# Kernel tuning notes

Measured on AMD Instinct MI355X. Metric: run time of the kernel, lower is better.

## Reference

```python
import jax, jax.numpy as jnp
import numpy as np
import math


def _instance_norm(x, eps=1e-5):
    # x: [B,C,H,W], normalize over spatial dims per (b,c)
    mu = jnp.mean(x, axis=(2, 3), keepdims=True)
    var = jnp.var(x, axis=(2, 3), keepdims=True)
    return (x - mu) * jax.lax.rsqrt(var + eps)


def _conv1x1(x, W, b):
    # x: [B,C,H,W], W: [O,C], b: [O]
    return jnp.einsum('oc,bchw->bohw', W, x) + b[None, :, None, None]


def setup_inputs() -> dict:
    key = jax.random.key(0)
    ks = jax.random.split(key, 17)
    B, C, H, W = 4, 256, 128, 128
    x = jax.random.normal(ks[0], (B, C, H, W), jnp.float32)
    def w(k):
        return jax.random.normal(k, (C, C), jnp.float32) * 0.02
    def bias(k):
        return jax.random.normal(k, (C,), jnp.float32) * 0.02
    return {
        'x': x,
        'Wq1': w(ks[1]), 'bq1': bias(ks[2]),
        'Wq2': w(ks[3]), 'bq2': bias(ks[4]),
        'Wk1': w(ks[5]), 'bk1': bias(ks[6]),
        'Wk2': w(ks[7]), 'bk2': bias(ks[8]),
        'Wv': w(ks[9]), 'bv': bias(ks[10]),
        'Wg': w(ks[11]), 'bg': bias(ks[12]),
        'Wo': w(ks[13]), 'bo': bias(ks[14]),
    }


def reference(x, Wq1, bq1, Wq2, bq2, Wk1, bk1, Wk2, bk2, Wv, bv, Wg, bg, Wo, bo):
    B, C, H, W = x.shape
    N = H * W
    sqrtC = math.sqrt(C)

    xn = _instance_norm(x)
    gelu = lambda t: jax.nn.gelu(t, approximate=False)

    q = jax.nn.softplus(_conv1x1(gelu(_conv1x1(xn, Wq1, bq1)), Wq2, bq2))
    k = jax.nn.softplus(_conv1x1(gelu(_conv1x1(xn, Wk1, bk1)), Wk2, bk2))
    v = gelu(_conv1x1(xn, Wv, bv))
    g = gelu(_conv1x1(xn, Wg, bg))

    q = q.reshape(B, C, N).transpose(0, 2, 1)  # [B,N,C]
    k = k.reshape(B, C, N)                     # [B,C,N]
    v = v.reshape(B, C, N).transpose(0, 2, 1)  # [B,N,C]

    kv = jnp.einsum('bcn,bnd->bcd', k, v)               # [B,C,C]
    z = jnp.einsum('bnc,bc->bn', q, k.sum(axis=-1)) / sqrtC
    z = 1.0 / (z + N)                                   # [B,N]

    out = jnp.einsum('bnc,bcd->bnd', q, kv) / sqrtC + v  # [B,N,C]
    out = out * z[:, :, None]
    out = out.transpose(0, 2, 1).reshape(B, C, H, W)
    out = out * g
    out = _conv1x1(out, Wo, bo)
    return out
```

## Files before the change

### kernel.cpp

```cpp
#include <hip/hip_runtime.h>
#include <cstdint>
#include <cstddef>


#define DI __device__ __forceinline__

typedef __attribute__((ext_vector_type(8))) short bf16x8;
typedef __attribute__((ext_vector_type(4))) short bf16x4;
typedef __attribute__((ext_vector_type(4))) float f32x4;

static constexpr int Cc = 256;
static constexpr int NN = 16384;

DI float bf2f(short s){ unsigned int u = ((unsigned int)(unsigned short)s) << 16; float f; __builtin_memcpy(&f, &u, 4); return f; }
DI short f2bf(float f){ unsigned int u; __builtin_memcpy(&u, &f, 4); u += 0x7fffu + ((u >> 16) & 1u); return (short)(u >> 16); }

typedef __attribute__((address_space(1))) const unsigned int gu32;
typedef __attribute__((address_space(3))) unsigned int lu32;
DI void gload16(const short* g, short* l){
    __builtin_amdgcn_global_load_lds((gu32*)g, (lu32*)l, 16, 0, 0);
}

DI float geluf(float x){
    float zz = x * 0.70710678118654752f;
    float az = fabsf(zz);
    float t  = __builtin_amdgcn_rcpf(fmaf(0.3275911f, az, 1.0f));
    float p  = fmaf(fmaf(fmaf(fmaf(1.061405429f, t, -1.453152027f), t,
                   1.421413741f), t, -0.284496736f), t, 0.254829592f) * t;
    float e  = __expf(-az * az);
    float er = copysignf(1.0f - p * e, zz);
    return 0.5f * x * (1.0f + er);
}
DI float softplusf(float x){
    float e = __expf(-fabsf(x));
    return fmaxf(x, 0.0f) + __logf(1.0f + e);
}

__global__ __launch_bounds__(256) void tw_conv(
    const float* __restrict__ W0, const float* __restrict__ W1,
    const float* __restrict__ W2, const float* __restrict__ W3,
    const float* __restrict__ W4, const float* __restrict__ W5,
    const float* __restrict__ W6, short* __restrict__ dst)
{
    const float* srcs[7] = {W0, W1, W2, W3, W4, W5, W6};
    const float* W = srcs[blockIdx.y];
    short* d = dst + (size_t)blockIdx.y * 65536;
    int i = blockIdx.x * 256 + threadIdx.x;
    float4 v = *(const float4*)(W + (size_t)i * 4);
    bf16x4 pk = { f2bf(v.x), f2bf(v.y), f2bf(v.z), f2bf(v.w) };
    *(bf16x4*)(d + (size_t)i * 4) = pk;
}

__global__ __launch_bounds__(256) void t0_stats(const float* __restrict__ x,
                                                float* __restrict__ mu, float* __restrict__ rstd)
{
    int row = blockIdx.x;
    const float4* p = (const float4*)(x + (size_t)row * NN);
    float s = 0.f, ss = 0.f;
    for (int i = threadIdx.x; i < NN/4; i += 256){
        float4 v = p[i];
        s  += v.x + v.y + v.z + v.w;
        ss += v.x*v.x + v.y*v.y + v.z*v.z + v.w*v.w;
    }
    #pragma unroll
    for (int o = 32; o; o >>= 1){ s += __shfl_down(s, o); ss += __shfl_down(ss, o); }
    __shared__ float a0[4], a1[4];
    int w = threadIdx.x >> 6;
    if ((threadIdx.x & 63) == 0){ a0[w] = s; a1[w] = ss; }
    __syncthreads();
    if (threadIdx.x == 0){
        float S = a0[0]+a0[1]+a0[2]+a0[3], SS = a1[0]+a1[1]+a1[2]+a1[3];
        float m = S * (1.f/NN);
        float var = SS * (1.f/NN) - m*m;
        mu[row] = m;
        rstd[row] = rsqrtf(var + 1e-5f);
    }
}

__global__ __launch_bounds__(256) void t1_xnT(const float* __restrict__ x,
                                              const float* __restrict__ mu, const float* __restrict__ rstd,
                                              short* __restrict__ xnT)
{
    int n0 = blockIdx.x * 64, c0 = blockIdx.y * 64, b = blockIdx.z;
    __shared__ __align__(16) short lds[64*72];
    int t = threadIdx.x;
    #pragma unroll
    for (int i = 0; i < 4; i++){
        int idx = i*256 + t;
        int c  = idx >> 4;
        int n4 = idx & 15;
        int cg = b*Cc + c0 + c;
        float4 v = *(const float4*)(x + (size_t)cg*NN + n0 + n4*4);
        float m = mu[cg], rs = rstd[cg];
        int key = (c ^ (c >> 3)) & 7;
        int blk = (n4 >> 1) ^ key;
        bf16x4 pk = { f2bf((v.x-m)*rs), f2bf((v.y-m)*rs), f2bf((v.z-m)*rs), f2bf((v.w-m)*rs) };
        *(bf16x4*)(&lds[c*72 + blk*8 + (n4&1)*4]) = pk;
    }
    __syncthreads();
    #pragma unroll
    for (int i = 0; i < 2; i++){
        int idx = i*256 + t;
        int n  = idx >> 3;
        int c8 = idx & 7;
        bf16x8 pk;
        #pragma unroll
        for (int j = 0; j < 8; j++){
            int c = c8*8 + j;
            int key = (c ^ (c >> 3)) & 7;
            pk[j] = lds[c*72 + (((n >> 3) ^ key))*8 + (n & 7)];
        }
        *(bf16x8*)(xnT + ((size_t)(b*NN + n0 + n))*Cc + c0 + c8*8) = pk;
    }
}

__global__ __launch_bounds__(256) void t2_conv1(const short* __restrict__ xnT,
    const short* __restrict__ wbf,
    const float* __restrict__ bv, const float* __restrict__ bg,
    short* __restrict__ yvg)
{
    int n0 = blockIdx.x * 128;
    int stile = blockIdx.y;
    int b = blockIdx.z;
    int branch = 2 + (stile >> 1);
    const short* wb = wbf + (size_t)branch * 65536;
    const float* bs = (stile >> 1) ? bg : bv;
    int s0b = (stile & 1) * 128;
    int dcol = stile * 128;

    __shared__ __align__(16) short Al[128*32];
    __shared__ __align__(16) short Bl[128*32];
    int t = threadIdx.x, lane = t & 63, wid = t >> 6;
    int wm = (wid & 1) * 64, wn = (wid >> 1) * 64;
    int l15 = lane & 15, g = lane >> 4;
    int srow = wid*16 + (lane >> 2);
    int scol = (lane & 3) * 8;
    int sdst = wid*512 + lane*8;

    f32x4 acc[4][4];
    #pragma unroll
    for (int i=0;i<4;i++)
        #pragma unroll
        for (int j=0;j<4;j++){ acc[i][j][0]=0.f; acc[i][j][1]=0.f; acc[i][j][2]=0.f; acc[i][j][3]=0.f; }

    const short* xb = xnT + (size_t)(b*NN + n0) * Cc;

    for (int k0 = 0; k0 < 256; k0 += 32){
        __syncthreads();
        #pragma unroll
        for (int i = 0; i < 2; i++){
            gload16(xb + (size_t)(i*64 + srow)*Cc + k0 + scol, &Al[i*2048 + sdst]);
            gload16(wb + (size_t)(s0b + i*64 + srow)*Cc + k0 + scol, &Bl[i*2048 + sdst]);
        }
        __syncthreads();
        bf16x8 bfr[4];
        #pragma unroll
        for (int ni = 0; ni < 4; ni++) bfr[ni] = *(const bf16x8*)(&Bl[(wn + ni*16 + l15)*32 + g*8]);
        #pragma unroll
        for (int mi = 0; mi < 4; mi++){
            bf16x8 a = *(const bf16x8*)(&Al[(wm + mi*16 + l15)*32 + g*8]);
            #pragma unroll
            for (int ni = 0; ni < 4; ni++)
                acc[mi][ni] = __builtin_amdgcn_mfma_f32_16x16x32_bf16(a, bfr[ni], acc[mi][ni], 0, 0, 0);
        }
    }
    short* outb = yvg + (size_t)(b*NN + n0) * 512 + dcol;
    #pragma unroll
    for (int mi = 0; mi < 4; mi++)
        #pragma unroll
        for (int ni = 0; ni < 4; ni++){
            int coll = wn + ni*16 + l15;
            float bias = bs[s0b + coll];
            #pragma unroll
            for (int r = 0; r < 4; r++){
                int row = wm + mi*16 + g*4 + r;
                outb[(size_t)row*512 + coll] = f2bf(geluf(acc[mi][ni][r] + bias));
            }
        }
}

__global__ __launch_bounds__(256) void t23_fused(const short* __restrict__ xnT,
    const short* __restrict__ wbf,
    const float* __restrict__ bq1, const float* __restrict__ bk1,
    const float* __restrict__ bq2, const float* __restrict__ bk2,
    short* __restrict__ qkT, float* __restrict__ ksum)
{
    int n0 = blockIdx.x * 64;
    int branch = blockIdx.y;
    int b = blockIdx.z;
    const short* w1 = wbf + (size_t)branch * 65536;
    const short* w2 = wbf + (size_t)(4 + branch) * 65536;
    const float* bs1 = branch ? bk1 : bq1;
    const float* bs2 = branch ? bk2 : bq2;

    __shared__ __align__(16) short Al[64*32];
    __shared__ __align__(16) short Bl[256*32];
    __shared__ __align__(16) short Y1[64*264];
    int t = threadIdx.x, lane = t & 63, wid = t >> 6;
    int wn = wid * 64;
    int l15 = lane & 15, g = lane >> 4;
    int srowA = t >> 2, scolA = (t & 3) * 8, sdstA = t * 8;
    int srowB = wid*16 + (lane >> 2);
    int scolB = (lane & 3) * 8;
    int sdstB = wid*512 + lane*8;

    const short* xb = xnT + (size_t)(b*NN + n0) * Cc;

    f32x4 acc[4][4];
    #pragma unroll
    for (int i=0;i<4;i++)
        #pragma unroll
        for (int j=0;j<4;j++){ acc[i][j][0]=0.f; acc[i][j][1]=0.f; acc[i][j][2]=0.f; acc[i][j][3]=0.f; }

    for (int k0 = 0; k0 < 256; k0 += 32){
        __syncthreads();
        gload16(xb + (size_t)srowA*Cc + k0 + scolA, &Al[sdstA]);
        #pragma unroll
        for (int i = 0; i < 4; i++)
            gload16(w1 + (size_t)(i*64 + srowB)*Cc + k0 + scolB, &Bl[i*2048 + sdstB]);
        __syncthreads();
        bf16x8 bfr[4];
        #pragma unroll
        for (int ni = 0; ni < 4; ni++) bfr[ni] = *(const bf16x8*)(&Bl[(wn + ni*16 + l15)*32 + g*8]);
        #pragma unroll
        for (int mi = 0; mi < 4; mi++){
            bf16x8 a = *(const bf16x8*)(&Al[(mi*16 + l15)*32 + g*8]);
            #pragma unroll
            for (int ni = 0; ni < 4; ni++)
                acc[mi][ni] = __builtin_amdgcn_mfma_f32_16x16x32_bf16(a, bfr[ni], acc[mi][ni], 0, 0, 0);
        }
    }
    #pragma unroll
    for (int mi = 0; mi < 4; mi++)
        #pragma unroll
        for (int ni = 0; ni < 4; ni++){
            int coll = wn + ni*16 + l15;
            float bias = bs1[coll];
            #pragma unroll
            for (int r = 0; r < 4; r++){
                int row = mi*16 + g*4 + r;
                Y1[row*264 + coll] = f2bf(geluf(acc[mi][ni][r] + bias));
            }
        }

    f32x4 acc2[4][4];
    #pragma unroll
    for (int i=0;i<4;i++)
        #pragma unroll
        for (int j=0;j<4;j++){ acc2[i][j][0]=0.f; acc2[i][j][1]=0.f; acc2[i][j][2]=0.f; acc2[i][j][3]=0.f; }

    for (int k0 = 0; k0 < 256; k0 += 32){
        __syncthreads();
        #pragma unroll
        for (int i = 0; i < 4; i++)
            gload16(w2 + (size_t)(i*64 + srowB)*Cc + k0 + scolB, &Bl[i*2048 + sdstB]);
        __syncthreads();
        bf16x8 bfr[4];
        #pragma unroll
        for (int ni = 0; ni < 4; ni++) bfr[ni] = *(const bf16x8*)(&Bl[(wn + ni*16 + l15)*32 + g*8]);
        #pragma unroll
        for (int mi = 0; mi < 4; mi++){
            bf16x8 a = *(const bf16x8*)(&Y1[(mi*16 + l15)*264 + k0 + g*8]);
            #pragma unroll
            for (int ni = 0; ni < 4; ni++)
                acc2[mi][ni] = __builtin_amdgcn_mfma_f32_16x16x32_bf16(a, bfr[ni], acc2[mi][ni], 0, 0, 0);
        }
    }
    short* outb = qkT + (size_t)(b*NN + n0) * 512 + branch*256;
    float csum[4] = {0.f, 0.f, 0.f, 0.f};
    #pragma unroll
    for (int mi = 0; mi < 4; mi++)
        #pragma unroll
        for (int ni = 0; ni < 4; ni++){
            int coll = wn + ni*16 + l15;
            float bias = bs2[coll];
            #pragma unroll
            for (int r = 0; r < 4; r++){
                int row = mi*16 + g*4 + r;
                float val = softplusf(acc2[mi][ni][r] + bias);
                outb[(size_t)row*512 + coll] = f2bf(val);
                csum[ni] += val;
            }
        }
    if (branch == 1){
        #pragma unroll
        for (int ni = 0; ni < 4; ni++){
            float v = csum[ni];
            v += __shfl_xor(v, 16);
            v += __shfl_xor(v, 32);
            if (g == 0) atomicAdd(&ksum[b*Cc + wn + ni*16 + l15], v);
        }
    }
}

__global__ __launch_bounds__(256) void t3t_transpose(const short* __restrict__ qkT, const short* __restrict__ yvg,
                                                     short* __restrict__ kC, short* __restrict__ vC)
{
    int n0 = blockIdx.x * 64;
    int c0 = blockIdx.y * 64;
    int b  = blockIdx.z >> 1;
    int which = blockIdx.z & 1;
    const short* src; short* dst;
    if (which == 0){ src = qkT + (size_t)(b*NN + n0)*512 + 256 + c0; dst = kC + (size_t)(b*Cc + c0)*NN + n0; }
    else           { src = yvg + (size_t)(b*NN + n0)*512 +   0 + c0; dst = vC + (size_t)(b*Cc + c0)*NN + n0; }
    __shared__ __align__(16) short lds[64*72];
    int t = threadIdx.x;
    #pragma unroll
    for (int i = 0; i < 2; i++){
        int idx = i*256 + t;
        int n = idx >> 3, c8 = idx & 7;
        bf16x8 v = *(const bf16x8*)(src + (size_t)n*512 + c8*8);
        int key = (n ^ (n >> 3)) & 7;
        *(bf16x8*)(&lds[n*72 + (c8 ^ key)*8]) = v;
    }
    __syncthreads();
    #pragma unroll
    for (int i = 0; i < 2; i++){
        int idx = i*256 + t;
        int c = idx >> 3, n8 = idx & 7;
        bf16x8 pk;
        #pragma unroll
        for (int j = 0; j < 8; j++){
            int n = n8*8 + j;
            int key = (n ^ (n >> 3)) & 7;
            pk[j] = lds[n*72 + (((c >> 3) ^ key))*8 + (c & 7)];
        }
        *(bf16x8*)(dst + (size_t)c*NN + n8*8) = pk;
    }
}

__global__ __launch_bounds__(256) void t4_kv(const short* __restrict__ kC, const short* __restrict__ vC,
                                             float* __restrict__ kv)
{
    int m0 = blockIdx.x * 128;
    int d0 = blockIdx.y * 128;
    int b  = blockIdx.z >> 5;
    int nb = (blockIdx.z & 31) * 512;

    __shared__ __align__(16) short Al[128*32];
    __shared__ __align__(16) short Bl[128*32];
    int t = threadIdx.x, lane = t & 63, wid = t >> 6;
    int wm = (wid & 1) * 64, wn = (wid >> 1) * 64;
    int l15 = lane & 15, g = lane >> 4;
    int srow = wid*16 + (lane >> 2);
    int scol = (lane & 3) * 8;
    int sdst = wid*512 + lane*8;

    f32x4 acc[4][4];
    #pragma unroll
    for (int i=0;i<4;i++)
        #pragma unroll
        for (int j=0;j<4;j++){ acc[i][j][0]=0.f; acc[i][j][1]=0.f; acc[i][j][2]=0.f; acc[i][j][3]=0.f; }

    const short* ka = kC + (size_t)(b*Cc + m0)*NN + nb;
    const short* vb = vC + (size_t)(b*Cc + d0)*NN + nb;

    for (int k0 = 0; k0 < 512; k0 += 32){
        __syncthreads();
        #pragma unroll
        for (int i = 0; i < 2; i++){
            gload16(ka + (size_t)(i*64 + srow)*NN + k0 + scol, &Al[i*2048 + sdst]);
            gload16(vb + (size_t)(i*64 + srow)*NN + k0 + scol, &Bl[i*2048 + sdst]);
        }
        __syncthreads();
        bf16x8 bfr[4];
        #pragma unroll
        for (int ni = 0; ni < 4; ni++) bfr[ni] = *(const bf16x8*)(&Bl[(wn + ni*16 + l15)*32 + g*8]);
        #pragma unroll
        for (int mi = 0; mi < 4; mi++){
            bf16x8 a = *(const bf16x8*)(&Al[(wm + mi*16 + l15)*32 + g*8]);
            #pragma unroll
            for (int ni = 0; ni < 4; ni++)
                acc[mi][ni] = __builtin_amdgcn_mfma_f32_16x16x32_bf16(a, bfr[ni], acc[mi][ni], 0, 0, 0);
        }
    }
    #pragma unroll
    for (int mi = 0; mi < 4; mi++)
        #pragma unroll
        for (int ni = 0; ni < 4; ni++){
            int coll = wn + ni*16 + l15;
            #pragma unroll
            for (int r = 0; r < 4; r++){
                int row = wm + mi*16 + g*4 + r;
                atomicAdd(&kv[((size_t)b*Cc + m0 + row)*Cc + d0 + coll], acc[mi][ni][r]);
            }
        }
}

__global__ __launch_bounds__(256) void t4c_kvT(const float* __restrict__ kv, short* __restrict__ kvT16)
{
    int d = blockIdx.x, b = blockIdx.y, c = threadIdx.x;
    float v = kv[((size_t)b*Cc + c)*Cc + d] * 0.0625f;
    kvT16[((size_t)b*Cc + d)*Cc + c] = f2bf(v);
}

__global__ __launch_bounds__(256) void t5_z(const short* __restrict__ qkT, const float* __restrict__ ksum,
                                            float* __restrict__ z)
{
    int b = blockIdx.y;
    int n0 = blockIdx.x * 32;
    __shared__ float ks[256];
    int t = threadIdx.x;
    ks[t] = ksum[b*Cc + t];
    __syncthreads();
    int row = n0 + (t >> 3), l8 = t & 7;
    const short* q = qkT + (size_t)(b*NN + row)*512;
    float acc = 0.f;
    #pragma unroll
    for (int i = 0; i < 4; i++){
        int c8 = i*8 + l8;
        bf16x8 v = *(const bf16x8*)(q + c8*8);
        #pragma unroll
        for (int j = 0; j < 8; j++) acc += bf2f(v[j]) * ks[c8*8 + j];
    }
    acc += __shfl_down(acc, 4, 8);
    acc += __shfl_down(acc, 2, 8);
    acc += __shfl_down(acc, 1, 8);
    if (l8 == 0) z[b*NN + row] = 1.0f / (acc * 0.0625f + 16384.0f);
}

__global__ __launch_bounds__(256) void t6_final(const short* __restrict__ qkT, const short* __restrict__ kvT16,
    const short* __restrict__ yvg, const float* __restrict__ z,
    const short* __restrict__ wbf, const float* __restrict__ bo, float* __restrict__ out)
{
    int n0 = blockIdx.x * 64, b = blockIdx.y;
    __shared__ __align__(16) short Aq[64*32];
    __shared__ __align__(16) short Bw[256*32];
    __shared__ __align__(16) short S[64*264];
    int t = threadIdx.x, lane = t & 63, wid = t >> 6;
    int l15 = lane & 15, g = lane >> 4;
    const short* wo_bf = wbf + (size_t)6 * 65536;
    int srow = wid*16 + (lane >> 2);
    int scol = (lane & 3) * 8;
    int sdst = wid*512 + lane*8;

    f32x4 acc[4][4];
    #pragma unroll
    for (int i=0;i<4;i++)
        #pragma unroll
        for (int j=0;j<4;j++){ acc[i][j][0]=0.f; acc[i][j][1]=0.f; acc[i][j][2]=0.f; acc[i][j][3]=0.f; }

    const short* qb = qkT + (size_t)(b*NN + n0)*512;
    const short* kvb = kvT16 + (size_t)b*Cc*Cc;

    for (int k0 = 0; k0 < 256; k0 += 32){
        __syncthreads();
        gload16(qb + (size_t)srow*512 + k0 + scol, &Aq[sdst]);
        #pragma unroll
        for (int i = 0; i < 4; i++)
            gload16(kvb + (size_t)(i*64 + srow)*Cc + k0 + scol, &Bw[i*2048 + sdst]);
        __syncthreads();
        bf16x8 bfr[4];
        #pragma unroll
        for (int ni = 0; ni < 4; ni++) bfr[ni] = *(const bf16x8*)(&Bw[(wid*64 + ni*16 + l15)*32 + g*8]);
        #pragma unroll
        for (int mi = 0; mi < 4; mi++){
            bf16x8 a = *(const bf16x8*)(&Aq[(mi*16 + l15)*32 + g*8]);
            #pragma unroll
            for (int ni = 0; ni < 4; ni++)
                acc[mi][ni] = __builtin_amdgcn_mfma_f32_16x16x32_bf16(a, bfr[ni], acc[mi][ni], 0, 0, 0);
        }
    }
    #pragma unroll
    for (int mi = 0; mi < 4; mi++)
        #pragma unroll
        for (int r = 0; r < 4; r++){
            int nl = mi*16 + g*4 + r;
            float zv = z[b*NN + n0 + nl];
            const short* vrow = yvg + (size_t)(b*NN + n0 + nl)*512;
            #pragma unroll
            for (int ni = 0; ni < 4; ni++){
                int d = wid*64 + ni*16 + l15;
                float vv = bf2f(vrow[d]);
                float gg = bf2f(vrow[256 + d]);
                S[nl*264 + d] = f2bf((acc[mi][ni][r] + vv) * zv * gg);
            }
        }
    __syncthreads();

    f32x4 acc2[4][4];
    #pragma unroll
    for (int i=0;i<4;i++)
        #pragma unroll
        for (int j=0;j<4;j++){ acc2[i][j][0]=0.f; acc2[i][j][1]=0.f; acc2[i][j][2]=0.f; acc2[i][j][3]=0.f; }

    for (int k0 = 0; k0 < 256; k0 += 32){
        __syncthreads();
        #pragma unroll
        for (int i = 0; i < 4; i++)
            gload16(wo_bf + (size_t)(i*64 + srow)*Cc + k0 + scol, &Bw[i*2048 + sdst]);
        __syncthreads();
        bf16x8 sfr[4];
        #pragma unroll
        for (int ni = 0; ni < 4; ni++) sfr[ni] = *(const bf16x8*)(&S[(ni*16 + l15)*264 + k0 + g*8]);
        #pragma unroll
        for (int mi = 0; mi < 4; mi++){
            bf16x8 a = *(const bf16x8*)(&Bw[(wid*64 + mi*16 + l15)*32 + g*8]);
            #pragma unroll
            for (int ni = 0; ni < 4; ni++)
                acc2[mi][ni] = __builtin_amdgcn_mfma_f32_16x16x32_bf16(a, sfr[ni], acc2[mi][ni], 0, 0, 0);
        }
    }
    #pragma unroll
    for (int mi = 0; mi < 4; mi++)
        #pragma unroll
        for (int ni = 0; ni < 4; ni++){
            int n = n0 + ni*16 + l15;
            #pragma unroll
            for (int r = 0; r < 4; r++){
                int o = wid*64 + mi*16 + g*4 + r;
                out[((size_t)b*Cc + o)*NN + n] = acc2[mi][ni][r] + bo[o];
            }
        }
}

extern "C" void kernel_launch(void* const* d_in, const int* in_sizes, int n_in,
                              void* d_out, int out_size, void* d_ws, size_t ws_size,
                              hipStream_t stream)
{
    (void)in_sizes; (void)n_in; (void)out_size; (void)ws_size;
    const float* x   = (const float*)d_in[0];
    const float* Wq1 = (const float*)d_in[1];
    const float* bq1 = (const float*)d_in[2];
    const float* Wq2 = (const float*)d_in[3];
    const float* bq2 = (const float*)d_in[4];
    const float* Wk1 = (const float*)d_in[5];
    const float* bk1 = (const float*)d_in[6];
    const float* Wk2 = (const float*)d_in[7];
    const float* bk2 = (const float*)d_in[8];
    const float* Wv  = (const float*)d_in[9];
    const float* bv  = (const float*)d_in[10];
    const float* Wg  = (const float*)d_in[11];
    const float* bg  = (const float*)d_in[12];
    const float* Wo  = (const float*)d_in[13];
    const float* bo  = (const float*)d_in[14];
    float* out = (float*)d_out;

    char* ws = (char*)d_ws;
    float* mu    = (float*)(ws + 0);
    float* rstd  = (float*)(ws + 4096);
    float* z     = (float*)(ws + 8192);
    short* kvT16 = (short*)(ws + 270336);
    short* wbf   = (short*)(ws + 794624);
    float* ksum  = (float*)(ws + 1712128);
    float* kv    = (float*)(ws + 1716224);
    short* xnT   = (short*)(ws + 3145728);
    short* kC    = (short*)(ws + 36700160);
    short* vC    = (short*)(ws + 70254592);
    short* yvg   = (short*)(ws + 103809024);
    short* qkT   = (short*)(ws + 170917888);

    hipMemsetAsync(ws + 1712128, 0, 4096 + 1048576, stream);

    tw_conv      <<<dim3(64, 7),      256, 0, stream>>>(Wq1, Wk1, Wv, Wg, Wq2, Wk2, Wo, wbf);
    t0_stats     <<<dim3(1024),       256, 0, stream>>>(x, mu, rstd);
    t1_xnT       <<<dim3(256, 4, 4),  256, 0, stream>>>(x, mu, rstd, xnT);
    t2_conv1     <<<dim3(128, 4, 4),  256, 0, stream>>>(xnT, wbf, bv, bg, yvg);
    t23_fused    <<<dim3(256, 2, 4),  256, 0, stream>>>(xnT, wbf, bq1, bk1, bq2, bk2, qkT, ksum);
    t3t_transpose<<<dim3(256, 4, 8),  256, 0, stream>>>(qkT, yvg, kC, vC);
    t4_kv        <<<dim3(2, 2, 128),  256, 0, stream>>>(kC, vC, kv);
    t4c_kvT      <<<dim3(256, 4),     256, 0, stream>>>(kv, kvT16);
    t5_z         <<<dim3(512, 4),     256, 0, stream>>>(qkT, ksum, z);
    t6_final     <<<dim3(256, 4),     256, 0, stream>>>(qkT, kvT16, yvg, z, wbf, bo, out);
}
```

Baseline: 409.2 us.

## Stage GEMM epilogues through LDS for coalesced stores; replace kv atomics with partial reduction

```diff
diff --git a/kernel.cpp b/kernel.cpp
--- a/kernel.cpp
+++ b/kernel.cpp
@@ -130,6 +130,7 @@
 
     __shared__ __align__(16) short Al[128*32];
     __shared__ __align__(16) short Bl[128*32];
+    __shared__ __align__(16) short Tsc[128*66];
     int t = threadIdx.x, lane = t & 63, wid = t >> 6;
     int wm = (wid & 1) * 64, wn = (wid >> 1) * 64;
     int l15 = lane & 15, g = lane >> 4;
@@ -166,17 +167,29 @@
     }
     short* outb = yvg + (size_t)(b*NN + n0) * 512 + dcol;
     #pragma unroll
-    for (int mi = 0; mi < 4; mi++)
-        #pragma unroll
-        for (int ni = 0; ni < 4; ni++){
-            int coll = wn + ni*16 + l15;
-            float bias = bs[s0b + coll];
-            #pragma unroll
-            for (int r = 0; r < 4; r++){
-                int row = wm + mi*16 + g*4 + r;
-                outb[(size_t)row*512 + coll] = f2bf(geluf(acc[mi][ni][r] + bias));
-            }
-        }
+    for (int h = 0; h < 2; h++){
+        __syncthreads();
+        if ((wid >> 1) == h){
+            #pragma unroll
+            for (int mi = 0; mi < 4; mi++)
+                #pragma unroll
+                for (int ni = 0; ni < 4; ni++){
+                    int cl = ni*16 + l15;
+                    float bias = bs[s0b + h*64 + cl];
+                    #pragma unroll
+                    for (int r = 0; r < 4; r++){
+                        int row = wm + mi*16 + g*4 + r;
+                        Tsc[row*66 + cl] = f2bf(geluf(acc[mi][ni][r] + bias));
+                    }
+                }
+        }
+        __syncthreads();
+        int row = t >> 1, seg = t & 1;
+        #pragma unroll
+        for (int j = 0; j < 4; j++)
+            *(bf16x8*)(outb + (size_t)row*512 + h*64 + seg*32 + j*8) =
+                *(const bf16x8*)(&Tsc[row*66 + seg*32 + j*8]);
+    }
 }
 
 __global__ __launch_bounds__(256) void t23_fused(const short* __restrict__ xnT,
@@ -266,7 +279,7 @@
                 acc2[mi][ni] = __builtin_amdgcn_mfma_f32_16x16x32_bf16(a, bfr[ni], acc2[mi][ni], 0, 0, 0);
         }
     }
-    short* outb = qkT + (size_t)(b*NN + n0) * 512 + branch*256;
+    __syncthreads();
     float csum[4] = {0.f, 0.f, 0.f, 0.f};
     #pragma unroll
     for (int mi = 0; mi < 4; mi++)
@@ -278,10 +291,19 @@
             for (int r = 0; r < 4; r++){
                 int row = mi*16 + g*4 + r;
                 float val = softplusf(acc2[mi][ni][r] + bias);
-                outb[(size_t)row*512 + coll] = f2bf(val);
+                Y1[row*264 + coll] = f2bf(val);
                 csum[ni] += val;
             }
         }
+    __syncthreads();
+    short* outb = qkT + (size_t)(b*NN + n0) * 512 + branch*256;
+    {
+        int row = t >> 2, cseg = (t & 3) * 64;
+        #pragma unroll
+        for (int j = 0; j < 8; j++)
+            *(bf16x8*)(outb + (size_t)row*512 + cseg + j*8) =
+                *(const bf16x8*)(&Y1[row*264 + cseg + j*8]);
+    }
     if (branch == 1){
         #pragma unroll
         for (int ni = 0; ni < 4; ni++){
@@ -330,12 +352,13 @@
 }
 
 __global__ __launch_bounds__(256) void t4_kv(const short* __restrict__ kC, const short* __restrict__ vC,
-                                             float* __restrict__ kv)
+                                             float* __restrict__ partial)
 {
     int m0 = blockIdx.x * 128;
     int d0 = blockIdx.y * 128;
     int b  = blockIdx.z >> 5;
-    int nb = (blockIdx.z & 31) * 512;
+    int s  = blockIdx.z & 31;
+    int nb = s * 512;
 
     __shared__ __align__(16) short Al[128*32];
     __shared__ __align__(16) short Bl[128*32];
@@ -374,6 +397,7 @@
                 acc[mi][ni] = __builtin_amdgcn_mfma_f32_16x16x32_bf16(a, bfr[ni], acc[mi][ni], 0, 0, 0);
         }
     }
+    float* pp = partial + (size_t)(s*4 + b) * 65536;
     #pragma unroll
     for (int mi = 0; mi < 4; mi++)
         #pragma unroll
@@ -382,16 +406,37 @@
             #pragma unroll
             for (int r = 0; r < 4; r++){
                 int row = wm + mi*16 + g*4 + r;
-                atomicAdd(&kv[((size_t)b*Cc + m0 + row)*Cc + d0 + coll], acc[mi][ni][r]);
+                pp[(size_t)(m0 + row)*Cc + d0 + coll] = acc[mi][ni][r];
             }
         }
 }
 
-__global__ __launch_bounds__(256) void t4c_kvT(const float* __restrict__ kv, short* __restrict__ kvT16)
-{
-    int d = blockIdx.x, b = blockIdx.y, c = threadIdx.x;
-    float v = kv[((size_t)b*Cc + c)*Cc + d] * 0.0625f;
-    kvT16[((size_t)b*Cc + d)*Cc + c] = f2bf(v);
+__global__ __launch_bounds__(256) void t4c_kvT(const float* __restrict__ partial, short* __restrict__ kvT16)
+{
+    int dt = blockIdx.x;
+    int b  = blockIdx.y;
+    __shared__ float L[256*17];
+    int t = threadIdx.x;
+    int dl = t & 15, cgrp = t >> 4;
+    #pragma unroll
+    for (int cc = 0; cc < 16; cc++){
+        int c = cc*16 + cgrp;
+        float sum = 0.f;
+        for (int s = 0; s < 32; s++)
+            sum += partial[(size_t)(s*4 + b)*65536 + (size_t)c*Cc + dt*16 + dl];
+        L[c*17 + dl] = sum * 0.0625f;
+    }
+    __syncthreads();
+    int d = t >> 4, c0 = (t & 15) * 16;
+    short* dst = kvT16 + ((size_t)b*Cc + dt*16 + d)*Cc + c0;
+    bf16x8 pk0, pk1;
+    #pragma unroll
+    for (int j = 0; j < 8; j++){
+        pk0[j] = f2bf(L[(c0 + j)*17 + d]);
+        pk1[j] = f2bf(L[(c0 + 8 + j)*17 + d]);
+    }
+    *(bf16x8*)(dst)     = pk0;
+    *(bf16x8*)(dst + 8) = pk1;
 }
 
 __global__ __launch_bounds__(256) void t5_z(const short* __restrict__ qkT, const float* __restrict__ ksum,
@@ -501,17 +546,32 @@
                 acc2[mi][ni] = __builtin_amdgcn_mfma_f32_16x16x32_bf16(a, sfr[ni], acc2[mi][ni], 0, 0, 0);
         }
     }
-    #pragma unroll
-    for (int mi = 0; mi < 4; mi++)
-        #pragma unroll
-        for (int ni = 0; ni < 4; ni++){
-            int n = n0 + ni*16 + l15;
-            #pragma unroll
-            for (int r = 0; r < 4; r++){
-                int o = wid*64 + mi*16 + g*4 + r;
-                out[((size_t)b*Cc + o)*NN + n] = acc2[mi][ni][r] + bo[o];
-            }
-        }
+    float* S32 = (float*)S;
+    #pragma unroll
+    for (int h = 0; h < 2; h++){
+        __syncthreads();
+        if ((wid >> 1) == h){
+            #pragma unroll
+            for (int mi = 0; mi < 4; mi++)
+                #pragma unroll
+                for (int ni = 0; ni < 4; ni++){
+                    #pragma unroll
+                    for (int r = 0; r < 4; r++){
+                        int o = wid*64 + mi*16 + g*4 + r;
+                        S32[(o & 127)*66 + ni*16 + l15] = acc2[mi][ni][r] + bo[o];
+                    }
+                }
+        }
+        __syncthreads();
+        int ol = t >> 1, seg = t & 1;
+        float* orow = out + ((size_t)b*Cc + h*128 + ol)*NN + n0 + seg*32;
+        #pragma unroll
+        for (int j = 0; j < 8; j++){
+            float4 v = { S32[ol*66 + seg*32 + j*4 + 0], S32[ol*66 + seg*32 + j*4 + 1],
+                         S32[ol*66 + seg*32 + j*4 + 2], S32[ol*66 + seg*32 + j*4 + 3] };
+            *(float4*)(orow + j*4) = v;
+        }
+    }
 }
 
 extern "C" void kernel_launch(void* const* d_in, const int* in_sizes, int n_in,
@@ -543,14 +603,14 @@
     short* kvT16 = (short*)(ws + 270336);
     short* wbf   = (short*)(ws + 794624);
     float* ksum  = (float*)(ws + 1712128);
-    float* kv    = (float*)(ws + 1716224);
     short* xnT   = (short*)(ws + 3145728);
+    float* partial = (float*)(ws + 3145728);
     short* kC    = (short*)(ws + 36700160);
     short* vC    = (short*)(ws + 70254592);
     short* yvg   = (short*)(ws + 103809024);
     short* qkT   = (short*)(ws + 170917888);
 
-    hipMemsetAsync(ws + 1712128, 0, 4096 + 1048576, stream);
+    hipMemsetAsync(ws + 1712128, 0, 4096, stream);
 
     tw_conv      <<<dim3(64, 7),      256, 0, stream>>>(Wq1, Wk1, Wv, Wg, Wq2, Wk2, Wo, wbf);
     t0_stats     <<<dim3(1024),       256, 0, stream>>>(x, mu, rstd);
@@ -558,8 +618,8 @@
     t2_conv1     <<<dim3(128, 4, 4),  256, 0, stream>>>(xnT, wbf, bv, bg, yvg);
     t23_fused    <<<dim3(256, 2, 4),  256, 0, stream>>>(xnT, wbf, bq1, bk1, bq2, bk2, qkT, ksum);
     t3t_transpose<<<dim3(256, 4, 8),  256, 0, stream>>>(qkT, yvg, kC, vC);
-    t4_kv        <<<dim3(2, 2, 128),  256, 0, stream>>>(kC, vC, kv);
-    t4c_kvT      <<<dim3(256, 4),     256, 0, stream>>>(kv, kvT16);
+    t4_kv        <<<dim3(2, 2, 128),  256, 0, stream>>>(kC, vC, partial);
+    t4c_kvT      <<<dim3(16, 4),      256, 0, stream>>>(partial, kvT16);
     t5_z         <<<dim3(512, 4),     256, 0, stream>>>(qkT, ksum, z);
     t6_final     <<<dim3(256, 4),     256, 0, stream>>>(qkT, kvT16, yvg, z, wbf, bo, out);
 }
```

Result: slower. 564.6 us (+38.0%).
